# Performance work log

Hardware: AMD Instinct MI355X
Metric: run time of the kernel (lower is better)

## Reference

```python
import jax, jax.numpy as jnp
import numpy as np

N_NODES = 100000
N_EDGES = 1600000
IN_DIM = 128
OUT_DIM = 64


def setup_inputs() -> dict:
    key = jax.random.key(0)
    k1, k2, k3, k4, k5 = jax.random.split(key, 5)
    return {
        "h_init": jax.random.normal(k1, (N_NODES, IN_DIM), dtype=jnp.float32),
        "W1": jax.random.normal(k2, (OUT_DIM, IN_DIM), dtype=jnp.float32),
        "a": jax.random.normal(k3, (1, OUT_DIM), dtype=jnp.float32),
        "src": jax.random.randint(k4, (N_EDGES,), 0, N_NODES, dtype=jnp.int64)
        if jax.config.jax_enable_x64 else jax.random.randint(k4, (N_EDGES,), 0, N_NODES, dtype=jnp.int32),
        "dst": jax.random.randint(k5, (N_EDGES,), 0, N_NODES, dtype=jnp.int32),
    }


def reference(h_init, W1, a, src, dst):
    N = h_init.shape[0]
    # node projection: [N, out_dim]
    h = h_init @ W1.T
    # per-edge diff feature: dst minus src (DGL edges.dst['h'] - edges.src['h'])
    diff = h[dst] - h[src]                       # [E, out_dim]
    e = jnp.tanh(diff @ a[0])                    # [E] edge attention logit
    # segment softmax over incoming edges of each destination node
    seg_max = jax.ops.segment_max(e, dst, num_segments=N)   # [N]
    ex = jnp.exp(e - seg_max[dst])               # [E]
    denom = jax.ops.segment_sum(ex, dst, num_segments=N)    # [N]
    alpha = ex / denom[dst]                      # [E]
    # weighted sum of diff features per destination node
    h_diff = jax.ops.segment_sum(alpha[:, None] * diff, dst, num_segments=N)  # [N, out_dim]
    return jax.nn.relu(h + h_diff)
```

## Files before the change

kernel.cpp:

```cpp
#include <hip/hip_runtime.h>
#include <hip/hip_fp16.h>

#define N_NODES 100000
#define N_EDGES 1600000
#define IN_DIM 128
#define OUT_DIM 64

#define NBUCK 391
#define BIN_NBLK 250
#define BIN_CHUNK 6400
#define MAXB 4608

#define PROJ_BLKS 1563

typedef short short8 __attribute__((ext_vector_type(8)));
typedef float f32x4 __attribute__((ext_vector_type(4)));

__device__ __forceinline__ short bf16_trunc(float x) {
  return (short)(__float_as_uint(x) >> 16);
}
__device__ __forceinline__ float bf16_tof(short s) {
  return __uint_as_float(((unsigned)(unsigned short)s) << 16);
}
__device__ __forceinline__ float edge_ex(float p) {
  float t2 = __expf(2.f * p);
  float th = 1.f - 2.f * __builtin_amdgcn_rcpf(t2 + 1.f);
  return __expf(th);
}

__global__ __launch_bounds__(256) void fat1_kernel(
    const float* __restrict__ h_init, const float* __restrict__ W1,
    const float* __restrict__ a, float* __restrict__ h,
    __half* __restrict__ h16, float* __restrict__ ha,
    int* __restrict__ bucket_cursor) {
  __shared__ short whi[16 * 64 * 8];
  __shared__ short wlo[16 * 64 * 8];

  if (blockIdx.x >= PROJ_BLKS) {
    for (int i = threadIdx.x; i < NBUCK; i += 256) bucket_cursor[i] = i * MAXB;
    return;
  }

  for (int idx = threadIdx.x; idx < 16 * 64; idx += 256) {
    int f = idx >> 6;
    int l = idx & 63;
    int kc = f >> 2, ot = f & 3;
    const float* wsrc =
        W1 + (ot * 16 + (l & 15)) * IN_DIM + kc * 32 + (l >> 4) * 8;
    short hi[8], lo[8];
#pragma unroll
    for (int j = 0; j < 8; j++) {
      float x = wsrc[j];
      short hv = bf16_trunc(x);
      hi[j] = hv;
      lo[j] = bf16_trunc(x - bf16_tof(hv));
    }
    *(short8*)&whi[idx * 8] = *(const short8*)hi;
    *(short8*)&wlo[idx * 8] = *(const short8*)lo;
  }

  int row0 = blockIdx.x * 64;
  int w = threadIdx.x >> 6;
  int l = threadIdx.x & 63;
  int m = l & 15;
  int q = l >> 4;

  int arow = row0 + w * 16 + m;
  if (arow >= N_NODES) arow = N_NODES - 1;
  const float* xsrc = h_init + (size_t)arow * IN_DIM + q * 8;

  short8 ahi[4], alo[4];
#pragma unroll
  for (int kc = 0; kc < 4; kc++) {
    float xv[8];
    *(float4*)&xv[0] = *(const float4*)(xsrc + kc * 32);
    *(float4*)&xv[4] = *(const float4*)(xsrc + kc * 32 + 4);
    short hi[8], lo[8];
#pragma unroll
    for (int j = 0; j < 8; j++) {
      short hv = bf16_trunc(xv[j]);
      hi[j] = hv;
      lo[j] = bf16_trunc(xv[j] - bf16_tof(hv));
    }
    ahi[kc] = *(const short8*)hi;
    alo[kc] = *(const short8*)lo;
  }
  __syncthreads();

  f32x4 acc[4] = {{0.f, 0.f, 0.f, 0.f},
                  {0.f, 0.f, 0.f, 0.f},
                  {0.f, 0.f, 0.f, 0.f},
                  {0.f, 0.f, 0.f, 0.f}};

#pragma unroll
  for (int kc = 0; kc < 4; kc++) {
#pragma unroll
    for (int ot = 0; ot < 4; ot++) {
      int base = (((kc << 2) | ot) * 64 + l) * 8;
      short8 bhi = *(const short8*)&whi[base];
      short8 blo = *(const short8*)&wlo[base];
      acc[ot] = __builtin_amdgcn_mfma_f32_16x16x32_bf16(ahi[kc], bhi, acc[ot],
                                                        0, 0, 0);
      acc[ot] = __builtin_amdgcn_mfma_f32_16x16x32_bf16(ahi[kc], blo, acc[ot],
                                                        0, 0, 0);
      acc[ot] = __builtin_amdgcn_mfma_f32_16x16x32_bf16(alo[kc], bhi, acc[ot],
                                                        0, 0, 0);
    }
  }

  float pa[4] = {0.f, 0.f, 0.f, 0.f};
#pragma unroll
  for (int ot = 0; ot < 4; ot++) {
    float aval = a[ot * 16 + m];
#pragma unroll
    for (int r = 0; r < 4; r++) pa[r] += acc[ot][r] * aval;
  }
  int rowb = row0 + w * 16 + q * 4;
#pragma unroll
  for (int r = 0; r < 4; r++) {
    int row = rowb + r;
    if (row < N_NODES) {
#pragma unroll
      for (int ot = 0; ot < 4; ot++) {
        h[(size_t)row * OUT_DIM + ot * 16 + m] = acc[ot][r];
        h16[(size_t)row * OUT_DIM + ot * 16 + m] = __float2half(acc[ot][r]);
      }
    }
  }
#pragma unroll
  for (int r = 0; r < 4; r++) {
    pa[r] += __shfl_xor(pa[r], 1);
    pa[r] += __shfl_xor(pa[r], 2);
    pa[r] += __shfl_xor(pa[r], 4);
    pa[r] += __shfl_xor(pa[r], 8);
  }
  if (m == 0) {
#pragma unroll
    for (int r = 0; r < 4; r++) {
      int row = rowb + r;
      if (row < N_NODES) ha[row] = pa[r];
    }
  }
}

__global__ __launch_bounds__(256) void bin_scatter_kernel(
    const int* __restrict__ src, const int* __restrict__ dst,
    int* __restrict__ bucket_cursor, unsigned int* __restrict__ pairs) {
  __shared__ int hst[NBUCK];
  __shared__ int cur[NBUCK];
  for (int i = threadIdx.x; i < NBUCK; i += 256) hst[i] = 0;
  __syncthreads();
  int beg = blockIdx.x * BIN_CHUNK;
  int end = min(beg + BIN_CHUNK, N_EDGES);
  for (int e = beg + threadIdx.x; e < end; e += 256)
    atomicAdd(&hst[dst[e] >> 8], 1);
  __syncthreads();
  for (int i = threadIdx.x; i < NBUCK; i += 256) {
    int c = hst[i];
    cur[i] = (c > 0) ? atomicAdd(&bucket_cursor[i], c) : 0;
  }
  __syncthreads();
  for (int e = beg + threadIdx.x; e < end; e += 256) {
    int d = dst[e];
    int pos = atomicAdd(&cur[d >> 8], 1);
    pairs[pos] = ((unsigned int)src[e] << 8) | (unsigned int)(d & 255);
  }
}

__global__ __launch_bounds__(256) void bucket_sort_kernel(
    const unsigned int* __restrict__ pairs,
    const int* __restrict__ bucket_cursor, const float* __restrict__ ha,
    int* __restrict__ nbeg, int* __restrict__ nend, int2* __restrict__ sorted) {
  __shared__ unsigned int plds[MAXB];
  __shared__ int hist[256];
  __shared__ int excl[256];
  __shared__ float had[256];
  int b = blockIdx.x;
  int t = threadIdx.x;
  int pbeg = b * MAXB;
  int pend = bucket_cursor[b];
  int cnt = pend - pbeg;

  int node = (b << 8) + t;
  had[t] = (node < N_NODES) ? ha[node] : 0.f;
  hist[t] = 0;
  __syncthreads();

  for (int i = t; i < cnt; i += 256) {
    unsigned int p = pairs[pbeg + i];
    plds[i] = p;
    atomicAdd(&hist[p & 255u], 1);
  }
  __syncthreads();

  int v = hist[t];
  excl[t] = v;
  __syncthreads();
  for (int off = 1; off < 256; off <<= 1) {
    int u = (t >= off) ? excl[t - off] : 0;
    __syncthreads();
    excl[t] += u;
    __syncthreads();
  }
  int my_excl = excl[t] - v;
  if (node < N_NODES) {
    nbeg[node] = pbeg + my_excl;
    nend[node] = pbeg + my_excl + v;
  }
  __syncthreads();
  hist[t] = my_excl;
  __syncthreads();

  for (int i = t; i < cnt; i += 256) {
    unsigned int p = plds[i];
    int d = (int)(p & 255u);
    int s = (int)(p >> 8);
    int pos = atomicAdd(&hist[d], 1);
    float ex = edge_ex(had[d] - ha[s]);
    sorted[pbeg + pos] = make_int2(s << 7, __float_as_int(ex));
  }
}

__global__ __launch_bounds__(256) void gather_kernel(
    const float* __restrict__ h, const __half* __restrict__ h16,
    const int* __restrict__ nbeg, const int* __restrict__ nend,
    const int2* __restrict__ sorted, float* __restrict__ out) {
  int wave = (blockIdx.x * 256 + threadIdx.x) >> 6;
  int lane = threadIdx.x & 63;
  if (wave >= N_NODES) return;
  int n = wave;
  int beg = nbeg[n];
  int end = nend[n];
  int g = lane >> 3;
  int l8 = lane & 7;

  const float4* h4 = (const float4*)h;
  float4 hd0 = h4[(size_t)n * (OUT_DIM / 4) + l8 * 2];
  float4 hd1 = h4[(size_t)n * (OUT_DIM / 4) + l8 * 2 + 1];

  const char* h16b = (const char*)h16;
  float acc[8] = {0.f, 0.f, 0.f, 0.f, 0.f, 0.f, 0.f, 0.f};
  float den = 0.f;

  for (int base = beg + g * 4; base < end; base += 32) {
    int last = end - 1;
    int2 e[4];
    float exv[4];
#pragma unroll
    for (int k = 0; k < 4; k++) {
      int i = base + k;
      e[k] = sorted[i < end ? i : last];
      exv[k] = (i < end) ? __int_as_float(e[k].y) : 0.f;
    }
    uint4 uv[4];
#pragma unroll
    for (int k = 0; k < 4; k++)
      uv[k] = *(const uint4*)(h16b + e[k].x + (l8 << 4));
#pragma unroll
    for (int k = 0; k < 4; k++) {
      union {
        uint4 u;
        __half hh[8];
      } U;
      U.u = uv[k];
      float ex = exv[k];
      den += ex;
#pragma unroll
      for (int j = 0; j < 8; j++)
        acc[j] = fmaf(__half2float(U.hh[j]), ex, acc[j]);
    }
  }

#pragma unroll
  for (int j = 0; j < 8; j++) {
    acc[j] += __shfl_xor(acc[j], 8);
    acc[j] += __shfl_xor(acc[j], 16);
    acc[j] += __shfl_xor(acc[j], 32);
  }
  den += __shfl_xor(den, 8);
  den += __shfl_xor(den, 16);
  den += __shfl_xor(den, 32);

  if (g == 0) {
    bool has = den > 0.f;
    float inv = has ? __builtin_amdgcn_rcpf(den) : 0.f;
    float4 r0, r1;
    r0.x = fmaxf(has ? 2.f * hd0.x - acc[0] * inv : hd0.x, 0.f);
    r0.y = fmaxf(has ? 2.f * hd0.y - acc[1] * inv : hd0.y, 0.f);
    r0.z = fmaxf(has ? 2.f * hd0.z - acc[2] * inv : hd0.z, 0.f);
    r0.w = fmaxf(has ? 2.f * hd0.w - acc[3] * inv : hd0.w, 0.f);
    r1.x = fmaxf(has ? 2.f * hd1.x - acc[4] * inv : hd1.x, 0.f);
    r1.y = fmaxf(has ? 2.f * hd1.y - acc[5] * inv : hd1.y, 0.f);
    r1.z = fmaxf(has ? 2.f * hd1.z - acc[6] * inv : hd1.z, 0.f);
    r1.w = fmaxf(has ? 2.f * hd1.w - acc[7] * inv : hd1.w, 0.f);
    float4* o4 = (float4*)out;
    o4[(size_t)n * (OUT_DIM / 4) + l8 * 2] = r0;
    o4[(size_t)n * (OUT_DIM / 4) + l8 * 2 + 1] = r1;
  }
}

extern "C" void kernel_launch(void* const* d_in, const int* in_sizes, int n_in,
                              void* d_out, int out_size, void* d_ws,
                              size_t ws_size, hipStream_t stream) {
  const float* h_init = (const float*)d_in[0];
  const float* W1 = (const float*)d_in[1];
  const float* a = (const float*)d_in[2];
  const int* src = (const int*)d_in[3];
  const int* dst = (const int*)d_in[4];
  float* out = (float*)d_out;

  float* h = (float*)d_ws;
  __half* h16 = (__half*)(h + (size_t)N_NODES * OUT_DIM);
  float* ha = (float*)(h16 + (size_t)N_NODES * OUT_DIM);
  unsigned int* pairs = (unsigned int*)(ha + N_NODES);
  int2* sorted = (int2*)(pairs + (size_t)NBUCK * MAXB);
  int* nbeg = (int*)(sorted + (size_t)NBUCK * MAXB);
  int* nend = nbeg + N_NODES;
  int* bucket_cursor = nend + N_NODES;

  fat1_kernel<<<PROJ_BLKS + 1, 256, 0, stream>>>(h_init, W1, a, h, h16, ha,
                                                 bucket_cursor);
  bin_scatter_kernel<<<BIN_NBLK, 256, 0, stream>>>(src, dst, bucket_cursor,
                                                   pairs);
  bucket_sort_kernel<<<NBUCK, 256, 0, stream>>>(pairs, bucket_cursor, ha, nbeg,
                                                nend, sorted);
  gather_kernel<<<(N_NODES * 64 + 255) / 256, 256, 0, stream>>>(
      h, h16, nbeg, nend, sorted, out);
}
```

Measured before the change: 207.6 us.

## Fuse edge binning into projection kernel and widen bucket sort blocks

Result: faster. 203.1 us (-2.2%).

```diff
diff --git a/kernel.cpp b/kernel.cpp
--- a/kernel.cpp
+++ b/kernel.cpp
@@ -7,11 +7,12 @@
 #define OUT_DIM 64
 
 #define NBUCK 391
-#define BIN_NBLK 250
-#define BIN_CHUNK 6400
+#define BIN_NBLK 800
+#define BIN_CHUNK 2000
 #define MAXB 4608
 
 #define PROJ_BLKS 1563
+#define SORT_THREADS 1024
 
 typedef short short8 __attribute__((ext_vector_type(8)));
 typedef float f32x4 __attribute__((ext_vector_type(4)));
@@ -30,16 +31,38 @@
 
 __global__ __launch_bounds__(256) void fat1_kernel(
     const float* __restrict__ h_init, const float* __restrict__ W1,
-    const float* __restrict__ a, float* __restrict__ h,
+    const float* __restrict__ a, const int* __restrict__ src,
+    const int* __restrict__ dst, float* __restrict__ h,
     __half* __restrict__ h16, float* __restrict__ ha,
-    int* __restrict__ bucket_cursor) {
-  __shared__ short whi[16 * 64 * 8];
-  __shared__ short wlo[16 * 64 * 8];
-
-  if (blockIdx.x >= PROJ_BLKS) {
-    for (int i = threadIdx.x; i < NBUCK; i += 256) bucket_cursor[i] = i * MAXB;
+    int* __restrict__ bucket_cursor, unsigned int* __restrict__ pairs) {
+  __shared__ __align__(16) char smem[16 * 64 * 8 * 2 * sizeof(short)];
+
+  if (blockIdx.x < BIN_NBLK) {
+    int* hst = (int*)smem;
+    int* cur = hst + NBUCK;
+    for (int i = threadIdx.x; i < NBUCK; i += 256) hst[i] = 0;
+    __syncthreads();
+    int beg = blockIdx.x * BIN_CHUNK;
+    int end = min(beg + BIN_CHUNK, N_EDGES);
+    for (int e = beg + threadIdx.x; e < end; e += 256)
+      atomicAdd(&hst[dst[e] >> 8], 1);
+    __syncthreads();
+    for (int i = threadIdx.x; i < NBUCK; i += 256) {
+      int c = hst[i];
+      cur[i] = (c > 0) ? atomicAdd(&bucket_cursor[i], c) + i * MAXB : 0;
+    }
+    __syncthreads();
+    for (int e = beg + threadIdx.x; e < end; e += 256) {
+      int d = dst[e];
+      int pos = atomicAdd(&cur[d >> 8], 1);
+      pairs[pos] = ((unsigned int)src[e] << 8) | (unsigned int)(d & 255);
+    }
     return;
   }
+
+  int pb = blockIdx.x - BIN_NBLK;
+  short* whi = (short*)smem;
+  short* wlo = whi + 16 * 64 * 8;
 
   for (int idx = threadIdx.x; idx < 16 * 64; idx += 256) {
     int f = idx >> 6;
@@ -59,7 +82,7 @@
     *(short8*)&wlo[idx * 8] = *(const short8*)lo;
   }
 
-  int row0 = blockIdx.x * 64;
+  int row0 = pb * 64;
   int w = threadIdx.x >> 6;
   int l = threadIdx.x & 63;
   int m = l & 15;
@@ -143,31 +166,7 @@
   }
 }
 
-__global__ __launch_bounds__(256) void bin_scatter_kernel(
-    const int* __restrict__ src, const int* __restrict__ dst,
-    int* __restrict__ bucket_cursor, unsigned int* __restrict__ pairs) {
-  __shared__ int hst[NBUCK];
-  __shared__ int cur[NBUCK];
-  for (int i = threadIdx.x; i < NBUCK; i += 256) hst[i] = 0;
-  __syncthreads();
-  int beg = blockIdx.x * BIN_CHUNK;
-  int end = min(beg + BIN_CHUNK, N_EDGES);
-  for (int e = beg + threadIdx.x; e < end; e += 256)
-    atomicAdd(&hst[dst[e] >> 8], 1);
-  __syncthreads();
-  for (int i = threadIdx.x; i < NBUCK; i += 256) {
-    int c = hst[i];
-    cur[i] = (c > 0) ? atomicAdd(&bucket_cursor[i], c) : 0;
-  }
-  __syncthreads();
-  for (int e = beg + threadIdx.x; e < end; e += 256) {
-    int d = dst[e];
-    int pos = atomicAdd(&cur[d >> 8], 1);
-    pairs[pos] = ((unsigned int)src[e] << 8) | (unsigned int)(d & 255);
-  }
-}
-
-__global__ __launch_bounds__(256) void bucket_sort_kernel(
+__global__ __launch_bounds__(SORT_THREADS) void bucket_sort_kernel(
     const unsigned int* __restrict__ pairs,
     const int* __restrict__ bucket_cursor, const float* __restrict__ ha,
     int* __restrict__ nbeg, int* __restrict__ nend, int2* __restrict__ sorted) {
@@ -178,40 +177,46 @@
   int b = blockIdx.x;
   int t = threadIdx.x;
   int pbeg = b * MAXB;
-  int pend = bucket_cursor[b];
-  int cnt = pend - pbeg;
-
-  int node = (b << 8) + t;
-  had[t] = (node < N_NODES) ? ha[node] : 0.f;
-  hist[t] = 0;
-  __syncthreads();
-
-  for (int i = t; i < cnt; i += 256) {
+  int cnt = bucket_cursor[b];
+
+  if (t < 256) {
+    int node = (b << 8) + t;
+    had[t] = (node < N_NODES) ? ha[node] : 0.f;
+    hist[t] = 0;
+  }
+  __syncthreads();
+
+  for (int i = t; i < cnt; i += SORT_THREADS) {
     unsigned int p = pairs[pbeg + i];
     plds[i] = p;
     atomicAdd(&hist[p & 255u], 1);
   }
   __syncthreads();
 
-  int v = hist[t];
-  excl[t] = v;
+  int v = 0;
+  if (t < 256) {
+    v = hist[t];
+    excl[t] = v;
+  }
   __syncthreads();
   for (int off = 1; off < 256; off <<= 1) {
-    int u = (t >= off) ? excl[t - off] : 0;
-    __syncthreads();
-    excl[t] += u;
-    __syncthreads();
-  }
-  int my_excl = excl[t] - v;
-  if (node < N_NODES) {
-    nbeg[node] = pbeg + my_excl;
-    nend[node] = pbeg + my_excl + v;
-  }
-  __syncthreads();
-  hist[t] = my_excl;
-  __syncthreads();
-
-  for (int i = t; i < cnt; i += 256) {
+    int u = (t >= off && t < 256) ? excl[t - off] : 0;
+    __syncthreads();
+    if (t < 256) excl[t] += u;
+    __syncthreads();
+  }
+  if (t < 256) {
+    int my_excl = excl[t] - v;
+    int node = (b << 8) + t;
+    if (node < N_NODES) {
+      nbeg[node] = pbeg + my_excl;
+      nend[node] = pbeg + my_excl + v;
+    }
+    hist[t] = my_excl;
+  }
+  __syncthreads();
+
+  for (int i = t; i < cnt; i += SORT_THREADS) {
     unsigned int p = plds[i];
     int d = (int)(p & 255u);
     int s = (int)(p >> 8);
@@ -318,12 +323,11 @@
   int* nend = nbeg + N_NODES;
   int* bucket_cursor = nend + N_NODES;
 
-  fat1_kernel<<<PROJ_BLKS + 1, 256, 0, stream>>>(h_init, W1, a, h, h16, ha,
-                                                 bucket_cursor);
-  bin_scatter_kernel<<<BIN_NBLK, 256, 0, stream>>>(src, dst, bucket_cursor,
-                                                   pairs);
-  bucket_sort_kernel<<<NBUCK, 256, 0, stream>>>(pairs, bucket_cursor, ha, nbeg,
-                                                nend, sorted);
+  hipMemsetAsync(bucket_cursor, 0, NBUCK * sizeof(int), stream);
+  fat1_kernel<<<BIN_NBLK + PROJ_BLKS, 256, 0, stream>>>(
+      h_init, W1, a, src, dst, h, h16, ha, bucket_cursor, pairs);
+  bucket_sort_kernel<<<NBUCK, SORT_THREADS, 0, stream>>>(
+      pairs, bucket_cursor, ha, nbeg, nend, sorted);
   gather_kernel<<<(N_NODES * 64 + 255) / 256, 256, 0, stream>>>(
       h, h16, nbeg, nend, sorted, out);
 }
```

## Replace bucketed two-pass sort with degree histogram, prefix scan and atomic scatter

Applied to the files above, without the earlier changes.

Result: slower. 308.5 us (+48.6%).

```diff
diff --git a/kernel.cpp b/kernel.cpp
--- a/kernel.cpp
+++ b/kernel.cpp
@@ -6,12 +6,15 @@
 #define IN_DIM 128
 #define OUT_DIM 64
 
-#define NBUCK 391
-#define BIN_NBLK 250
-#define BIN_CHUNK 6400
-#define MAXB 4608
-
 #define PROJ_BLKS 1563
+#define HIST_NBLK 400
+#define HIST_CHUNK 4000
+
+#define SCAN_BLK 1024
+#define SCAN_NBLK 98
+
+#define SCAT_EPT 4
+#define SCAT_NBLK ((N_EDGES / SCAT_EPT + 255) / 256)
 
 typedef short short8 __attribute__((ext_vector_type(8)));
 typedef float f32x4 __attribute__((ext_vector_type(4)));
@@ -30,16 +33,26 @@
 
 __global__ __launch_bounds__(256) void fat1_kernel(
     const float* __restrict__ h_init, const float* __restrict__ W1,
-    const float* __restrict__ a, float* __restrict__ h,
-    __half* __restrict__ h16, float* __restrict__ ha,
-    int* __restrict__ bucket_cursor) {
+    const float* __restrict__ a, const int* __restrict__ dst,
+    float* __restrict__ h, __half* __restrict__ h16, float* __restrict__ ha,
+    int* __restrict__ deg) {
   __shared__ short whi[16 * 64 * 8];
   __shared__ short wlo[16 * 64 * 8];
 
-  if (blockIdx.x >= PROJ_BLKS) {
-    for (int i = threadIdx.x; i < NBUCK; i += 256) bucket_cursor[i] = i * MAXB;
+  if (blockIdx.x < HIST_NBLK) {
+    int beg = blockIdx.x * HIST_CHUNK;
+    int end = beg + HIST_CHUNK;
+    for (int e = beg + threadIdx.x * 4; e + 3 < end; e += 256 * 4) {
+      int4 d4 = *(const int4*)&dst[e];
+      atomicAdd(&deg[d4.x], 1);
+      atomicAdd(&deg[d4.y], 1);
+      atomicAdd(&deg[d4.z], 1);
+      atomicAdd(&deg[d4.w], 1);
+    }
     return;
   }
+
+  int pb = blockIdx.x - HIST_NBLK;
 
   for (int idx = threadIdx.x; idx < 16 * 64; idx += 256) {
     int f = idx >> 6;
@@ -59,7 +72,7 @@
     *(short8*)&wlo[idx * 8] = *(const short8*)lo;
   }
 
-  int row0 = blockIdx.x * 64;
+  int row0 = pb * 64;
   int w = threadIdx.x >> 6;
   int l = threadIdx.x & 63;
   int m = l & 15;
@@ -143,81 +156,66 @@
   }
 }
 
-__global__ __launch_bounds__(256) void bin_scatter_kernel(
+__global__ __launch_bounds__(SCAN_BLK) void scan1_kernel(
+    const int* __restrict__ deg, int* __restrict__ nbeg,
+    int* __restrict__ bsum) {
+  __shared__ int sc[SCAN_BLK];
+  int t = threadIdx.x;
+  int i = blockIdx.x * SCAN_BLK + t;
+  int v = (i < N_NODES) ? deg[i] : 0;
+  sc[t] = v;
+  __syncthreads();
+  for (int off = 1; off < SCAN_BLK; off <<= 1) {
+    int u = (t >= off) ? sc[t - off] : 0;
+    __syncthreads();
+    sc[t] += u;
+    __syncthreads();
+  }
+  if (i < N_NODES) nbeg[i] = sc[t] - v;
+  if (t == SCAN_BLK - 1) bsum[blockIdx.x] = sc[t];
+}
+
+__global__ __launch_bounds__(SCAN_BLK) void scan2_kernel(
+    const int* __restrict__ deg, const int* __restrict__ bsum,
+    int* __restrict__ nbeg, int* __restrict__ nend, int* __restrict__ cursor) {
+  __shared__ int red[SCAN_BLK];
+  int t = threadIdx.x;
+  int b = blockIdx.x;
+  int part = (t < b) ? bsum[t] : 0;
+  red[t] = part;
+  __syncthreads();
+  for (int s = SCAN_BLK / 2; s > 0; s >>= 1) {
+    if (t < s) red[t] += red[t + s];
+    __syncthreads();
+  }
+  int off = red[0];
+  int i = b * SCAN_BLK + t;
+  if (i < N_NODES) {
+    int beg = off + nbeg[i];
+    int dv = deg[i];
+    nbeg[i] = beg;
+    nend[i] = beg + dv;
+    cursor[i] = beg;
+  }
+}
+
+__global__ __launch_bounds__(256) void scatter_kernel(
     const int* __restrict__ src, const int* __restrict__ dst,
-    int* __restrict__ bucket_cursor, unsigned int* __restrict__ pairs) {
-  __shared__ int hst[NBUCK];
-  __shared__ int cur[NBUCK];
-  for (int i = threadIdx.x; i < NBUCK; i += 256) hst[i] = 0;
-  __syncthreads();
-  int beg = blockIdx.x * BIN_CHUNK;
-  int end = min(beg + BIN_CHUNK, N_EDGES);
-  for (int e = beg + threadIdx.x; e < end; e += 256)
-    atomicAdd(&hst[dst[e] >> 8], 1);
-  __syncthreads();
-  for (int i = threadIdx.x; i < NBUCK; i += 256) {
-    int c = hst[i];
-    cur[i] = (c > 0) ? atomicAdd(&bucket_cursor[i], c) : 0;
-  }
-  __syncthreads();
-  for (int e = beg + threadIdx.x; e < end; e += 256) {
-    int d = dst[e];
-    int pos = atomicAdd(&cur[d >> 8], 1);
-    pairs[pos] = ((unsigned int)src[e] << 8) | (unsigned int)(d & 255);
-  }
-}
-
-__global__ __launch_bounds__(256) void bucket_sort_kernel(
-    const unsigned int* __restrict__ pairs,
-    const int* __restrict__ bucket_cursor, const float* __restrict__ ha,
-    int* __restrict__ nbeg, int* __restrict__ nend, int2* __restrict__ sorted) {
-  __shared__ unsigned int plds[MAXB];
-  __shared__ int hist[256];
-  __shared__ int excl[256];
-  __shared__ float had[256];
-  int b = blockIdx.x;
-  int t = threadIdx.x;
-  int pbeg = b * MAXB;
-  int pend = bucket_cursor[b];
-  int cnt = pend - pbeg;
-
-  int node = (b << 8) + t;
-  had[t] = (node < N_NODES) ? ha[node] : 0.f;
-  hist[t] = 0;
-  __syncthreads();
-
-  for (int i = t; i < cnt; i += 256) {
-    unsigned int p = pairs[pbeg + i];
-    plds[i] = p;
-    atomicAdd(&hist[p & 255u], 1);
-  }
-  __syncthreads();
-
-  int v = hist[t];
-  excl[t] = v;
-  __syncthreads();
-  for (int off = 1; off < 256; off <<= 1) {
-    int u = (t >= off) ? excl[t - off] : 0;
-    __syncthreads();
-    excl[t] += u;
-    __syncthreads();
-  }
-  int my_excl = excl[t] - v;
-  if (node < N_NODES) {
-    nbeg[node] = pbeg + my_excl;
-    nend[node] = pbeg + my_excl + v;
-  }
-  __syncthreads();
-  hist[t] = my_excl;
-  __syncthreads();
-
-  for (int i = t; i < cnt; i += 256) {
-    unsigned int p = plds[i];
-    int d = (int)(p & 255u);
-    int s = (int)(p >> 8);
-    int pos = atomicAdd(&hist[d], 1);
-    float ex = edge_ex(had[d] - ha[s]);
-    sorted[pbeg + pos] = make_int2(s << 7, __float_as_int(ex));
+    const float* __restrict__ ha, int* __restrict__ cursor,
+    int2* __restrict__ sorted) {
+  int e = (blockIdx.x * 256 + threadIdx.x) * SCAT_EPT;
+  if (e >= N_EDGES) return;
+  int4 s4 = *(const int4*)&src[e];
+  int4 d4 = *(const int4*)&dst[e];
+  int ss[4] = {s4.x, s4.y, s4.z, s4.w};
+  int dd[4] = {d4.x, d4.y, d4.z, d4.w};
+  float ex[4];
+#pragma unroll
+  for (int k = 0; k < 4; k++) ex[k] = edge_ex(ha[dd[k]] - ha[ss[k]]);
+#pragma unroll
+  for (int k = 0; k < 4; k++) {
+    int pos = atomicAdd(&cursor[dd[k]], 1);
+    sorted[pos] = make_int2(ss[k] << 7, __float_as_int(ex[k]));
   }
 }
 
@@ -312,18 +310,20 @@
   float* h = (float*)d_ws;
   __half* h16 = (__half*)(h + (size_t)N_NODES * OUT_DIM);
   float* ha = (float*)(h16 + (size_t)N_NODES * OUT_DIM);
-  unsigned int* pairs = (unsigned int*)(ha + N_NODES);
-  int2* sorted = (int2*)(pairs + (size_t)NBUCK * MAXB);
-  int* nbeg = (int*)(sorted + (size_t)NBUCK * MAXB);
+  int2* sorted = (int2*)(ha + N_NODES);
+  int* nbeg = (int*)(sorted + (size_t)N_EDGES);
   int* nend = nbeg + N_NODES;
-  int* bucket_cursor = nend + N_NODES;
-
-  fat1_kernel<<<PROJ_BLKS + 1, 256, 0, stream>>>(h_init, W1, a, h, h16, ha,
-                                                 bucket_cursor);
-  bin_scatter_kernel<<<BIN_NBLK, 256, 0, stream>>>(src, dst, bucket_cursor,
-                                                   pairs);
-  bucket_sort_kernel<<<NBUCK, 256, 0, stream>>>(pairs, bucket_cursor, ha, nbeg,
-                                                nend, sorted);
+  int* cursor = nend + N_NODES;
+  int* deg = cursor + N_NODES;
+  int* bsum = deg + N_NODES;
+
+  hipMemsetAsync(deg, 0, N_NODES * sizeof(int), stream);
+  fat1_kernel<<<HIST_NBLK + PROJ_BLKS, 256, 0, stream>>>(h_init, W1, a, dst, h,
+                                                         h16, ha, deg);
+  scan1_kernel<<<SCAN_NBLK, SCAN_BLK, 0, stream>>>(deg, nbeg, bsum);
+  scan2_kernel<<<SCAN_NBLK, SCAN_BLK, 0, stream>>>(deg, bsum, nbeg, nend,
+                                                   cursor);
+  scatter_kernel<<<SCAT_NBLK, 256, 0, stream>>>(src, dst, ha, cursor, sorted);
   gather_kernel<<<(N_NODES * 64 + 255) / 256, 256, 0, stream>>>(
       h, h16, nbeg, nend, sorted, out);
 }
```
